# Optimization experiments

Measured on AMD Instinct MI355X. Metric: run time of the kernel, lower is better.

## Reference

```python
import jax, jax.numpy as jnp
import numpy as np

B, C, T, H, W = 8, 512, 8, 28, 28
DI, DO = 256, 512  # dim_inner, dim_out
INIT_STD = 0.01
BN_EPS = 1e-5


def conv1x1(x, w, b):
    # 1x1x1 Conv3d == channel contraction. x: [B,C,T,H,W], w: [O,C], b: [O]
    return jnp.einsum('bcthw,oc->bothw', x, w) + b[None, :, None, None, None]


def setup_inputs() -> dict:
    key = jax.random.key(0)
    ks = jax.random.split(key, 8)
    x = jax.random.normal(ks[0], (B, C, T, H, W), jnp.float32)
    theta_w = INIT_STD * jax.random.normal(ks[1], (DI, C), jnp.float32)
    phi_w = INIT_STD * jax.random.normal(ks[2], (DI, C), jnp.float32)
    g_w = INIT_STD * jax.random.normal(ks[3], (DI, C), jnp.float32)
    out_w = INIT_STD * jax.random.normal(ks[4], (DO, DI), jnp.float32)
    theta_b = jnp.zeros((DI,), jnp.float32)
    phi_b = jnp.zeros((DI,), jnp.float32)
    g_b = jnp.zeros((DI,), jnp.float32)
    out_b = jnp.zeros((DO,), jnp.float32)
    bn_gamma = jnp.ones((DO,), jnp.float32)  # BN_INIT_GAMMA = 1.0
    bn_beta = jnp.zeros((DO,), jnp.float32)
    return {"x": x, "theta_w": theta_w, "theta_b": theta_b, "phi_w": phi_w,
            "phi_b": phi_b, "g_w": g_w, "g_b": g_b, "out_w": out_w,
            "out_b": out_b, "bn_gamma": bn_gamma, "bn_beta": bn_beta}


def reference(x, theta_w, theta_b, phi_w, phi_b, g_w, g_b, out_w, out_b, bn_gamma, bn_beta):
    b, c, t, h, w = x.shape
    scale = DI ** (-0.5)
    # theta on full resolution
    theta = conv1x1(x, theta_w, theta_b).reshape(b, DI, -1)          # [B,DI,N]
    # MaxPool3d((1,2,2)) with stride (1,2,2): H,W even -> block max
    mp = x.reshape(b, c, t, h // 2, 2, w // 2, 2).max(axis=(4, 6))   # [B,C,T,H/2,W/2]
    phi = conv1x1(mp, phi_w, phi_b).reshape(b, DI, -1)               # [B,DI,M]
    g = conv1x1(mp, g_w, g_b).reshape(b, DI, -1)                     # [B,DI,M]
    # attention: theta^T phi -> [B,N,M], scaled softmax over M
    logits = jnp.einsum('bdn,bdm->bnm', theta, phi) * scale
    p = jax.nn.softmax(logits, axis=-1)
    # t = g @ p^T -> [B,DI,N]
    tt = jnp.einsum('bdm,bnm->bdn', g, p).reshape(b, DI, t, h, w)
    out = conv1x1(tt, out_w, out_b)                                  # [B,DO,T,H,W]
    # BatchNorm3d (training-mode batch statistics over B,T,H,W)
    mean = out.mean(axis=(0, 2, 3, 4), keepdims=True)
    var = out.var(axis=(0, 2, 3, 4), keepdims=True)
    out = (out - mean) * jax.lax.rsqrt(var + BN_EPS)
    out = out * bn_gamma[None, :, None, None, None] + bn_beta[None, :, None, None, None]
    return out + x
```

## Files before the change

kernel.cpp:

```cpp
#include <hip/hip_runtime.h>
#include <hip/hip_bf16.h>

#define B_ 8
#define C_ 512
#define T_ 8
#define H_ 28
#define W_ 28
#define N_ (T_*H_*W_)
#define HP_ 14
#define WP_ 14
#define M_ (T_*HP_*WP_)
#define DI_ 256
#define DO_ 512
#define BN_EPS 1e-5f
#define SCALE_LOG2E 0.090168440055560214f
#define PSUM_COLS 392

typedef __attribute__((ext_vector_type(8))) short short8;
typedef __attribute__((ext_vector_type(4))) float float4v;
typedef __attribute__((ext_vector_type(16))) float float16v;
typedef __attribute__((ext_vector_type(2))) float float2v;

__device__ inline unsigned short f2bf(float f) {
    union { float f; unsigned int u; } v; v.f = f;
    unsigned int u = v.u;
    return (unsigned short)((u + 0x7FFFu + ((u >> 16) & 1u)) >> 16);
}
__device__ inline float bf2f(unsigned short h) {
    union { unsigned int u; float f; } v; v.u = ((unsigned int)h) << 16;
    return v.f;
}

__global__ void xpose_x(const float* __restrict__ x, unsigned short* __restrict__ xT) {
    __shared__ float tile[64][65];
    int b = blockIdx.z;
    int c0 = blockIdx.y * 64, n0 = blockIdx.x * 64;
    const float* src = x + (size_t)b * C_ * N_;
    int tx = threadIdx.x & 63, ty = threadIdx.x >> 6;
#pragma unroll
    for (int i = 0; i < 16; i++) {
        int c = ty + i * 4;
        tile[c][tx] = src[(size_t)(c0 + c) * N_ + n0 + tx];
    }
    __syncthreads();
    unsigned short* d = xT + ((size_t)b * N_ + n0) * C_ + c0;
#pragma unroll
    for (int i = 0; i < 16; i++) {
        int n = ty + i * 4;
        d[(size_t)n * C_ + tx] = f2bf(tile[tx][n]);
    }
}

__global__ void pool_xpose(const float* __restrict__ x, unsigned short* __restrict__ mpT) {
    __shared__ unsigned short tile[196][72];
    int b = blockIdx.z, t = blockIdx.y, c0 = blockIdx.x * 64;
    const float* src = x + (((size_t)b * C_ + c0) * T_ + t) * 784;
    for (int idx = threadIdx.x; idx < 64 * 196; idx += 256) {
        int cc = idx / 196, p = idx - cc * 196;
        int hp = p / 14, wp = p - hp * 14;
        const float* r0 = src + (size_t)cc * T_ * 784 + (2 * hp) * 28 + 2 * wp;
        float2v a = *(const float2v*)r0;
        float2v c = *(const float2v*)(r0 + 28);
        float m = fmaxf(fmaxf(a.x, a.y), fmaxf(c.x, c.y));
        tile[p][cc] = f2bf(m);
    }
    __syncthreads();
    unsigned short* d = mpT + ((size_t)b * M_ + t * 196) * C_ + c0;
    for (int idx = threadIdx.x; idx < 196 * 64; idx += 256) {
        int p = idx >> 6, cc = idx & 63;
        d[(size_t)p * C_ + cc] = tile[p][cc];
    }
}

__global__ void cast_w(const float* __restrict__ s, unsigned short* __restrict__ d, int n) {
    int i = blockIdx.x * 256 + threadIdx.x;
    if (i < n) d[i] = f2bf(s[i]);
}

template<int BIAS_MODE>
__global__ __launch_bounds__(256) void btgemm(
        const unsigned short* __restrict__ A, size_t strideAb,
        const unsigned short* __restrict__ Bm, size_t strideBb,
        unsigned short* __restrict__ Dp, size_t strideDb,
        const float* __restrict__ bias, int Mdim, int Ndim, int Kdim) {
    int b = blockIdx.z;
    const unsigned short* Ab = A + (size_t)b * strideAb;
    const unsigned short* Bb = Bm + (size_t)b * strideBb;
    int m0 = blockIdx.x * 64, n0 = blockIdx.y * 64;
    int wave = threadIdx.x >> 6, lane = threadIdx.x & 63;
    int wm = (wave >> 1) * 32, wn = (wave & 1) * 32;
    int lr = lane & 15, lk = lane >> 4;
    float4v acc[2][2] = {};
    for (int k0 = 0; k0 < Kdim; k0 += 32) {
        short8 a[2], bb[2];
#pragma unroll
        for (int i = 0; i < 2; i++) {
            int ar = m0 + wm + i * 16 + lr; if (ar >= Mdim) ar = Mdim - 1;
            a[i] = *(const short8*)(Ab + (size_t)ar * Kdim + k0 + lk * 8);
            int br = n0 + wn + i * 16 + lr; if (br >= Ndim) br = Ndim - 1;
            bb[i] = *(const short8*)(Bb + (size_t)br * Kdim + k0 + lk * 8);
        }
#pragma unroll
        for (int i = 0; i < 2; i++)
#pragma unroll
            for (int j = 0; j < 2; j++)
                acc[i][j] = __builtin_amdgcn_mfma_f32_16x16x32_bf16(a[i], bb[j], acc[i][j], 0, 0, 0);
    }
#pragma unroll
    for (int i = 0; i < 2; i++)
#pragma unroll
        for (int j = 0; j < 2; j++) {
            int col = n0 + wn + j * 16 + lr;
#pragma unroll
            for (int r = 0; r < 4; r++) {
                int row = m0 + wm + i * 16 + lk * 4 + r;
                if (row < Mdim && col < Ndim) {
                    float v = acc[i][j][r];
                    if (BIAS_MODE == 1) v += bias[col];
                    else if (BIAS_MODE == 2) v += bias[row];
                    Dp[(size_t)b * strideDb + (size_t)row * Ndim + col] = f2bf(v);
                }
            }
        }
}

__global__ __launch_bounds__(256, 2) void theta_gemm(
        const unsigned short* __restrict__ xT, const unsigned short* __restrict__ wq,
        unsigned short* __restrict__ thetaT, const float* __restrict__ bias) {
    __shared__ __align__(16) unsigned short wqs[2][32][512];
    const int bid = blockIdx.x;
    const int b = bid & 7;
    const int nblk = bid >> 3;
    const int wave = threadIdx.x >> 6, lane = threadIdx.x & 63;
    const int lr = lane & 15, lk = lane >> 4;
    const unsigned short* Ab = xT + ((size_t)b * N_ + nblk * 128 + wave * 32) * C_;

    short8 a[2][16];
#pragma unroll
    for (int i = 0; i < 2; i++)
#pragma unroll
        for (int kd = 0; kd < 16; kd++)
            a[i][kd] = *(const short8*)(Ab + (size_t)(i * 16 + lr) * C_ + kd * 32 + lk * 8);

    auto stage = [&](int bufi, int t) {
#pragma unroll
        for (int j = 0; j < 8; j++) {
            int row = wave * 8 + j;
            int qq = (lane * 16) ^ ((row & 7) << 4);
            const unsigned short* src = wq + (size_t)(t * 32 + row) * C_ + (qq >> 1);
            unsigned short* dst = &wqs[bufi][0][0] + row * 512;
            __builtin_amdgcn_global_load_lds(
                (const __attribute__((address_space(1))) unsigned int*)src,
                (__attribute__((address_space(3))) unsigned int*)dst, 16, 0, 0);
        }
    };

    stage(0, 0);
    const int hq = (lk * 16) ^ ((lr & 7) << 4);
    unsigned short* D = thetaT + ((size_t)b * N_ + nblk * 128 + wave * 32) * DI_;
    int buf = 0;
#pragma unroll
    for (int t = 0; t < 8; t++) {
        if (t < 7) {
            stage(buf ^ 1, t + 1);
            asm volatile("s_waitcnt vmcnt(8)" ::: "memory");
        } else {
            asm volatile("s_waitcnt vmcnt(0)" ::: "memory");
        }
        __syncthreads();
        const char* W = (const char*)&wqs[buf][0][0];
        float4v acc[2][2] = {};
#pragma unroll
        for (int kd = 0; kd < 16; kd++) {
            short8 b0 = *(const short8*)(W + lr * 1024 + ((kd * 64) ^ hq));
            short8 b1 = *(const short8*)(W + (16 + lr) * 1024 + ((kd * 64) ^ hq));
            acc[0][0] = __builtin_amdgcn_mfma_f32_16x16x32_bf16(a[0][kd], b0, acc[0][0], 0, 0, 0);
            acc[0][1] = __builtin_amdgcn_mfma_f32_16x16x32_bf16(a[0][kd], b1, acc[0][1], 0, 0, 0);
            acc[1][0] = __builtin_amdgcn_mfma_f32_16x16x32_bf16(a[1][kd], b0, acc[1][0], 0, 0, 0);
            acc[1][1] = __builtin_amdgcn_mfma_f32_16x16x32_bf16(a[1][kd], b1, acc[1][1], 0, 0, 0);
        }
#pragma unroll
        for (int i = 0; i < 2; i++)
#pragma unroll
            for (int j = 0; j < 2; j++) {
                int col = t * 32 + j * 16 + lr;
                float bv = bias[col];
#pragma unroll
                for (int r = 0; r < 4; r++) {
                    int row = i * 16 + lk * 4 + r;
                    D[(size_t)row * DI_ + col] = f2bf(acc[i][j][r] + bv);
                }
            }
        __syncthreads();
        buf ^= 1;
    }
}

__global__ __launch_bounds__(256, 2) void out_gemm(
        const unsigned short* __restrict__ wo,
        const unsigned short* __restrict__ Bh, const unsigned short* __restrict__ Bl,
        float* __restrict__ Dp, const float* __restrict__ bias,
        float* __restrict__ psum) {
    __shared__ __align__(16) unsigned short tts[2][2][32][256];
    const int bid = blockIdx.x;
    const int b = bid & 7;
    const int rem = bid >> 3;
    const int doblk = rem & 3;
    const int nchunk = rem >> 2;
    const int wave = threadIdx.x >> 6, lane = threadIdx.x & 63;
    const int lr = lane & 15, lk = lane >> 4;
    const unsigned short* Ab = wo + (size_t)(doblk * 128 + wave * 32) * DI_;
    const unsigned short* BhB = Bh + ((size_t)b * N_ + nchunk * 128) * DI_;
    const unsigned short* BlB = Bl + ((size_t)b * N_ + nchunk * 128) * DI_;

    short8 a[2][8];
#pragma unroll
    for (int i = 0; i < 2; i++)
#pragma unroll
        for (int kd = 0; kd < 8; kd++)
            a[i][kd] = *(const short8*)(Ab + (size_t)(i * 16 + lr) * DI_ + kd * 32 + lk * 8);

    auto stage = [&](int bufi, int t) {
#pragma unroll
        for (int p = 0; p < 2; p++) {
            const unsigned short* S = p ? BlB : BhB;
#pragma unroll
            for (int j = 0; j < 4; j++) {
                int chunk = wave * 4 + j;
                int row = chunk * 2 + (lane >> 5);
                int qq = (((lane & 31) * 16)) ^ ((row & 7) << 4);
                const unsigned short* src = S + (size_t)(t * 32 + row) * DI_ + (qq >> 1);
                unsigned short* dst = &tts[bufi][p][0][0] + chunk * 512;
                __builtin_amdgcn_global_load_lds(
                    (const __attribute__((address_space(1))) unsigned int*)src,
                    (__attribute__((address_space(3))) unsigned int*)dst, 16, 0, 0);
            }
        }
    };

    stage(0, 0);
    const int hq = (lk * 16) ^ ((lr & 7) << 4);
    float4v acc[4][2][2] = {};
    int buf = 0;
#pragma unroll
    for (int t = 0; t < 4; t++) {
        if (t < 3) {
            stage(buf ^ 1, t + 1);
            asm volatile("s_waitcnt vmcnt(8)" ::: "memory");
        } else {
            asm volatile("s_waitcnt vmcnt(0)" ::: "memory");
        }
        __syncthreads();
        const char* th = (const char*)&tts[buf][0][0][0];
        const char* tl = (const char*)&tts[buf][1][0][0];
#pragma unroll
        for (int kd = 0; kd < 8; kd++) {
            short8 bh0 = *(const short8*)(th + lr * 512 + ((kd * 64) ^ hq));
            short8 bh1 = *(const short8*)(th + (16 + lr) * 512 + ((kd * 64) ^ hq));
            short8 bl0 = *(const short8*)(tl + lr * 512 + ((kd * 64) ^ hq));
            short8 bl1 = *(const short8*)(tl + (16 + lr) * 512 + ((kd * 64) ^ hq));
            acc[t][0][0] = __builtin_amdgcn_mfma_f32_16x16x32_bf16(a[0][kd], bh0, acc[t][0][0], 0, 0, 0);
            acc[t][0][0] = __builtin_amdgcn_mfma_f32_16x16x32_bf16(a[0][kd], bl0, acc[t][0][0], 0, 0, 0);
            acc[t][0][1] = __builtin_amdgcn_mfma_f32_16x16x32_bf16(a[0][kd], bh1, acc[t][0][1], 0, 0, 0);
            acc[t][0][1] = __builtin_amdgcn_mfma_f32_16x16x32_bf16(a[0][kd], bl1, acc[t][0][1], 0, 0, 0);
            acc[t][1][0] = __builtin_amdgcn_mfma_f32_16x16x32_bf16(a[1][kd], bh0, acc[t][1][0], 0, 0, 0);
            acc[t][1][0] = __builtin_amdgcn_mfma_f32_16x16x32_bf16(a[1][kd], bl0, acc[t][1][0], 0, 0, 0);
            acc[t][1][1] = __builtin_amdgcn_mfma_f32_16x16x32_bf16(a[1][kd], bh1, acc[t][1][1], 0, 0, 0);
            acc[t][1][1] = __builtin_amdgcn_mfma_f32_16x16x32_bf16(a[1][kd], bl1, acc[t][1][1], 0, 0, 0);
        }
        __syncthreads();
        buf ^= 1;
    }
    float* Db = Dp + (size_t)b * DO_ * N_;
    float s1[2][4] = {}, s2[2][4] = {};
#pragma unroll
    for (int t = 0; t < 4; t++)
#pragma unroll
        for (int i = 0; i < 2; i++)
#pragma unroll
            for (int r = 0; r < 4; r++) {
                int dorow = doblk * 128 + wave * 32 + i * 16 + lk * 4 + r;
                float bv = bias[dorow];
                float v0 = acc[t][i][0][r] + bv;
                float v1 = acc[t][i][1][r] + bv;
                int ncol = nchunk * 128 + t * 32 + lr;
                Db[(size_t)dorow * N_ + ncol] = v0;
                Db[(size_t)dorow * N_ + ncol + 16] = v1;
                s1[i][r] += v0 + v1;
                s2[i][r] += v0 * v0 + v1 * v1;
            }
#pragma unroll
    for (int m = 1; m < 16; m <<= 1)
#pragma unroll
        for (int i = 0; i < 2; i++)
#pragma unroll
            for (int r = 0; r < 4; r++) {
                s1[i][r] += __shfl_xor(s1[i][r], m, 64);
                s2[i][r] += __shfl_xor(s2[i][r], m, 64);
            }
    if (lr == 0) {
        int pcol = b * 49 + nchunk;
#pragma unroll
        for (int i = 0; i < 2; i++)
#pragma unroll
            for (int r = 0; r < 4; r++) {
                int row = doblk * 128 + wave * 32 + i * 16 + lk * 4 + r;
                psum[(size_t)row * PSUM_COLS + pcol] = s1[i][r];
                psum[(size_t)(DO_ + row) * PSUM_COLS + pcol] = s2[i][r];
            }
    }
}

__global__ __launch_bounds__(256, 2) void attn_k(
        const unsigned short* __restrict__ thetaT,
        const unsigned short* __restrict__ phiT,
        const unsigned short* __restrict__ g,
        unsigned short* __restrict__ ttH,
        unsigned short* __restrict__ ttL) {
    __shared__ __align__(16) unsigned short phi_s[2][32][256];
    __shared__ __align__(16) unsigned short g_s[2][256][32];
    const int bid = blockIdx.x;
    const int b = bid & 7;
    const int nblk = bid >> 3;
    const int wave = threadIdx.x >> 6, lane = threadIdx.x & 63;
    const int l31 = lane & 31, hi = lane >> 5;
    const int n0 = nblk * 128 + wave * 32;
    const unsigned short* Q  = thetaT + ((size_t)b * N_ + n0) * DI_;
    const unsigned short* Pg = phiT + (size_t)b * M_ * DI_;
    const unsigned short* G  = g + (size_t)b * DI_ * M_;

    short8 q[16];
#pragma unroll
    for (int kb = 0; kb < 16; kb++)
        q[kb] = *(const short8*)(Q + (size_t)l31 * DI_ + kb * 16 + hi * 8);

    float16v acc[8] = {};
    float rs = 0.f;

    auto stage = [&](int bufi, int t) {
        const unsigned short* phiRow = Pg + (size_t)t * 32 * DI_;
#pragma unroll
        for (int j = 0; j < 4; j++) {
            int chunk = wave * 4 + j;
            int row = chunk * 2 + (lane >> 5);
            int qq = ((lane & 31) * 16) ^ ((row & 7) << 4);
            const unsigned short* src = phiRow + (size_t)row * DI_ + (qq >> 1);
            unsigned short* dst = &phi_s[bufi][0][0] + chunk * 512;
            __builtin_amdgcn_global_load_lds(
                (const __attribute__((address_space(1))) unsigned int*)src,
                (__attribute__((address_space(3))) unsigned int*)dst, 16, 0, 0);
        }
#pragma unroll
        for (int j = 0; j < 4; j++) {
            int chunk = wave * 4 + j;
            int d = chunk * 16 + (lane >> 2);
            int mq = (lane & 3) ^ ((lane >> 3) & 3);
            const unsigned short* src = G + (size_t)d * M_ + t * 32 + mq * 8;
            unsigned short* dst = &g_s[bufi][0][0] + chunk * 512;
            __builtin_amdgcn_global_load_lds(
                (const __attribute__((address_space(1))) unsigned int*)src,
                (__attribute__((address_space(3))) unsigned int*)dst, 16, 0, 0);
        }
    };

    stage(0, 0);
    const int pswz = (l31 & 7) << 4;
    const int gswz = ((lane >> 1) & 3) << 4;
    int buf = 0;
    const int NT = M_ / 32;
    for (int t = 0; t < NT; t++) {
        if (t + 1 < NT) {
            stage(buf ^ 1, t + 1);
            asm volatile("s_waitcnt vmcnt(8)" ::: "memory");
        } else {
            asm volatile("s_waitcnt vmcnt(0)" ::: "memory");
        }
        __syncthreads();

        const char* phiB = (const char*)&phi_s[buf][0][0];
        float16v S = {};
        __builtin_amdgcn_s_setprio(1);
#pragma unroll
        for (int kb = 0; kb < 16; kb++) {
            short8 pha = *(const short8*)(phiB + l31 * 512 + ((kb * 32 + hi * 16) ^ pswz));
            S = __builtin_amdgcn_mfma_f32_32x32x16_bf16(pha, q[kb], S, 0, 0, 0);
        }
        __builtin_amdgcn_s_setprio(0);

        float p[16];
#pragma unroll
        for (int r = 0; r < 16; r++) {
            p[r] = exp2f(S[r] * SCALE_LOG2E);
            rs += p[r];
        }
        unsigned int pk0, pk1, pk2, pk3, pk4, pk5, pk6, pk7;
        asm("v_cvt_pk_bf16_f32 %0, %1, %2" : "=v"(pk0) : "v"(p[0]),  "v"(p[1]));
        asm("v_cvt_pk_bf16_f32 %0, %1, %2" : "=v"(pk1) : "v"(p[2]),  "v"(p[3]));
        asm("v_cvt_pk_bf16_f32 %0, %1, %2" : "=v"(pk2) : "v"(p[4]),  "v"(p[5]));
        asm("v_cvt_pk_bf16_f32 %0, %1, %2" : "=v"(pk3) : "v"(p[6]),  "v"(p[7]));
        asm("v_cvt_pk_bf16_f32 %0, %1, %2" : "=v"(pk4) : "v"(p[8]),  "v"(p[9]));
        asm("v_cvt_pk_bf16_f32 %0, %1, %2" : "=v"(pk5) : "v"(p[10]), "v"(p[11]));
        asm("v_cvt_pk_bf16_f32 %0, %1, %2" : "=v"(pk6) : "v"(p[12]), "v"(p[13]));
        asm("v_cvt_pk_bf16_f32 %0, %1, %2" : "=v"(pk7) : "v"(p[14]), "v"(p[15]));
        asm("v_permlane32_swap_b32 %0, %1" : "+v"(pk0), "+v"(pk2));
        asm("v_permlane32_swap_b32 %0, %1" : "+v"(pk1), "+v"(pk3));
        asm("v_permlane32_swap_b32 %0, %1" : "+v"(pk4), "+v"(pk6));
        asm("v_permlane32_swap_b32 %0, %1" : "+v"(pk5), "+v"(pk7));
        union UF { unsigned int u[4]; short8 s; } pa0, pa1;
        pa0.u[0] = pk0; pa0.u[1] = pk1; pa0.u[2] = pk2; pa0.u[3] = pk3;
        pa1.u[0] = pk4; pa1.u[1] = pk5; pa1.u[2] = pk6; pa1.u[3] = pk7;

        const char* gB = (const char*)&g_s[buf][0][0];
        const int goff0 = (hi * 16) ^ gswz;
        const int goff1 = (32 + hi * 16) ^ gswz;
        __builtin_amdgcn_s_setprio(1);
#pragma unroll
        for (int dblk = 0; dblk < 8; dblk++) {
            short8 gb0 = *(const short8*)(gB + (dblk * 32 + l31) * 64 + goff0);
            short8 gb1 = *(const short8*)(gB + (dblk * 32 + l31) * 64 + goff1);
            acc[dblk] = __builtin_amdgcn_mfma_f32_32x32x16_bf16(pa0.s, gb0, acc[dblk], 0, 0, 0);
            acc[dblk] = __builtin_amdgcn_mfma_f32_32x32x16_bf16(pa1.s, gb1, acc[dblk], 0, 0, 0);
        }
        __builtin_amdgcn_s_setprio(0);
        __syncthreads();
        buf ^= 1;
    }

    rs += __shfl_xor(rs, 32, 64);
    float inv = 1.0f / rs;

    unsigned short* OH = ttH + ((size_t)b * N_ + n0) * DI_;
    unsigned short* OL = ttL + ((size_t)b * N_ + n0) * DI_;
#pragma unroll
    for (int reg = 0; reg < 16; reg++) {
        int n_l = (reg & 3) + 8 * (reg >> 2) + 4 * hi;
        float invn = __shfl(inv, n_l, 64);
#pragma unroll
        for (int dblk = 0; dblk < 8; dblk++) {
            float v = acc[dblk][reg] * invn;
            unsigned short h = f2bf(v);
            unsigned short l = f2bf(v - bf2f(h));
            size_t idx = (size_t)n_l * DI_ + dblk * 32 + l31;
            OH[idx] = h;
            OL[idx] = l;
        }
    }
}

__global__ void bn_finalize(const float* __restrict__ psum, float* __restrict__ stats) {
    int o = blockIdx.x;
    float s = 0.f, q = 0.f;
    for (int c = threadIdx.x; c < PSUM_COLS; c += 256) {
        s += psum[(size_t)o * PSUM_COLS + c];
        q += psum[(size_t)(DO_ + o) * PSUM_COLS + c];
    }
#pragma unroll
    for (int m = 1; m < 64; m <<= 1) { s += __shfl_xor(s, m, 64); q += __shfl_xor(q, m, 64); }
    __shared__ float ws1[4], ws2[4];
    int wave = threadIdx.x >> 6;
    if ((threadIdx.x & 63) == 0) { ws1[wave] = s; ws2[wave] = q; }
    __syncthreads();
    if (threadIdx.x == 0) {
        double S = (double)ws1[0] + ws1[1] + ws1[2] + ws1[3];
        double Q = (double)ws2[0] + ws2[1] + ws2[2] + ws2[3];
        const double cnt = (double)(B_ * N_);
        double mean = S / cnt;
        double var = Q / cnt - mean * mean;
        stats[o] = (float)mean;
        stats[DO_ + o] = (float)(1.0 / sqrt(var + (double)BN_EPS));
    }
}

__global__ void bn_apply(float* __restrict__ out, const float* __restrict__ x,
                         const float* __restrict__ stats, const float* __restrict__ gamma,
                         const float* __restrict__ beta) {
    size_t i = (size_t)blockIdx.x * 256 + threadIdx.x;
    float4v v = ((const float4v*)out)[i];
    float4v xv = ((const float4v*)x)[i];
    int o = (int)((i * 4 / N_) % DO_);
    float mean = stats[o], rsig = stats[DO_ + o];
    float ga = gamma[o], be = beta[o];
    float4v r;
#pragma unroll
    for (int j = 0; j < 4; j++) r[j] = (v[j] - mean) * rsig * ga + be + xv[j];
    ((float4v*)out)[i] = r;
}

extern "C" void kernel_launch(void* const* d_in, const int* in_sizes, int n_in,
                              void* d_out, int out_size, void* d_ws, size_t ws_size,
                              hipStream_t stream) {
    const float* x       = (const float*)d_in[0];
    const float* theta_w = (const float*)d_in[1];
    const float* theta_b = (const float*)d_in[2];
    const float* phi_w   = (const float*)d_in[3];
    const float* phi_b   = (const float*)d_in[4];
    const float* g_w     = (const float*)d_in[5];
    const float* g_b     = (const float*)d_in[6];
    const float* out_w   = (const float*)d_in[7];
    const float* out_b   = (const float*)d_in[8];
    const float* bn_g    = (const float*)d_in[9];
    const float* bn_b    = (const float*)d_in[10];
    float* out = (float*)d_out;

    char* ws = (char*)d_ws;
    size_t off = 0;
    auto alloc = [&](size_t bytes) { void* p = ws + off; off += (bytes + 255) & ~(size_t)255; return p; };
    unsigned short* xT     = (unsigned short*)alloc((size_t)B_ * N_ * C_ * 2);
    unsigned short* mpT    = (unsigned short*)alloc((size_t)B_ * M_ * C_ * 2);
    unsigned short* thetaT = (unsigned short*)alloc((size_t)B_ * N_ * DI_ * 2);
    unsigned short* phiT   = (unsigned short*)alloc((size_t)B_ * M_ * DI_ * 2);
    unsigned short* gbuf   = (unsigned short*)alloc((size_t)B_ * DI_ * M_ * 2);
    unsigned short* wq     = (unsigned short*)alloc((size_t)DI_ * C_ * 2);
    unsigned short* wp     = (unsigned short*)alloc((size_t)DI_ * C_ * 2);
    unsigned short* wg     = (unsigned short*)alloc((size_t)DI_ * C_ * 2);
    unsigned short* wo     = (unsigned short*)alloc((size_t)DO_ * DI_ * 2);
    float* stats           = (float*)alloc((size_t)DO_ * 2 * 4);
    float* psum            = (float*)alloc((size_t)DO_ * 2 * PSUM_COLS * 4);
    unsigned short* ttH    = xT;
    unsigned short* ttL    = xT + (size_t)B_ * N_ * DI_;

    cast_w<<<(DI_ * C_ + 255) / 256, 256, 0, stream>>>(theta_w, wq, DI_ * C_);
    cast_w<<<(DI_ * C_ + 255) / 256, 256, 0, stream>>>(phi_w, wp, DI_ * C_);
    cast_w<<<(DI_ * C_ + 255) / 256, 256, 0, stream>>>(g_w, wg, DI_ * C_);
    cast_w<<<(DO_ * DI_ + 255) / 256, 256, 0, stream>>>(out_w, wo, DO_ * DI_);

    xpose_x<<<dim3(N_ / 64, C_ / 64, B_), 256, 0, stream>>>(x, xT);
    pool_xpose<<<dim3(C_ / 64, T_, B_), 256, 0, stream>>>(x, mpT);

    theta_gemm<<<392, 256, 0, stream>>>(xT, wq, thetaT, theta_b);
    btgemm<1><<<dim3((M_ + 63) / 64, DI_ / 64, B_), 256, 0, stream>>>(
        mpT, (size_t)M_ * C_, wp, 0, phiT, (size_t)M_ * DI_, phi_b, M_, DI_, C_);
    btgemm<2><<<dim3(DI_ / 64, (M_ + 63) / 64, B_), 256, 0, stream>>>(
        wg, 0, mpT, (size_t)M_ * C_, gbuf, (size_t)DI_ * M_, g_b, DI_, M_, C_);

    attn_k<<<dim3((N_ / 128) * 8), 256, 0, stream>>>(thetaT, phiT, gbuf, ttH, ttL);

    out_gemm<<<1568, 256, 0, stream>>>(wo, ttH, ttL, out, out_b, psum);

    bn_finalize<<<DO_, 256, 0, stream>>>(psum, stats);
    bn_apply<<<(size_t)B_ * DO_ * N_ / 4 / 256, 256, 0, stream>>>(out, x, stats, bn_g, bn_b);
}
```

Measured before the change: 383.7 us.

## Replace syncthreads with raw barriers, relax vmcnt waits, split logits accumulator chain

Replaces __syncthreads with a bare s_barrier wrapped in compiler memory fences, which drops the implicit full waitcnt before each barrier. Because the theta GEMM's global stores then stay pending, its vmcnt thresholds are raised so those stores do not force waits. The attention kernel's QK^T MFMA chain is split into two independent accumulators that are summed before the exp. The goal is fewer pipeline stalls from barriers and serial MFMA dependencies. The risks are LDS hazards if the hand-tuned vmcnt counts are wrong, plus a few extra registers.

```diff
diff --git a/kernel.cpp b/kernel.cpp
--- a/kernel.cpp
+++ b/kernel.cpp
@@ -29,6 +29,11 @@
 __device__ inline float bf2f(unsigned short h) {
     union { unsigned int u; float f; } v; v.u = ((unsigned int)h) << 16;
     return v.f;
+}
+__device__ inline void blockbar() {
+    asm volatile("" ::: "memory");
+    __builtin_amdgcn_s_barrier();
+    asm volatile("" ::: "memory");
 }
 
 __global__ void xpose_x(const float* __restrict__ x, unsigned short* __restrict__ xT) {
@@ -163,11 +168,12 @@
     for (int t = 0; t < 8; t++) {
         if (t < 7) {
             stage(buf ^ 1, t + 1);
-            asm volatile("s_waitcnt vmcnt(8)" ::: "memory");
+            if (t == 0) asm volatile("s_waitcnt vmcnt(8)" ::: "memory");
+            else        asm volatile("s_waitcnt vmcnt(24)" ::: "memory");
         } else {
-            asm volatile("s_waitcnt vmcnt(0)" ::: "memory");
-        }
-        __syncthreads();
+            asm volatile("s_waitcnt vmcnt(16)" ::: "memory");
+        }
+        blockbar();
         const char* W = (const char*)&wqs[buf][0][0];
         float4v acc[2][2] = {};
 #pragma unroll
@@ -191,7 +197,7 @@
                     D[(size_t)row * DI_ + col] = f2bf(acc[i][j][r] + bv);
                 }
             }
-        __syncthreads();
+        blockbar();
         buf ^= 1;
     }
 }
@@ -250,7 +256,7 @@
         } else {
             asm volatile("s_waitcnt vmcnt(0)" ::: "memory");
         }
-        __syncthreads();
+        blockbar();
         const char* th = (const char*)&tts[buf][0][0][0];
         const char* tl = (const char*)&tts[buf][1][0][0];
 #pragma unroll
@@ -268,7 +274,7 @@
             acc[t][1][1] = __builtin_amdgcn_mfma_f32_16x16x32_bf16(a[1][kd], bh1, acc[t][1][1], 0, 0, 0);
             acc[t][1][1] = __builtin_amdgcn_mfma_f32_16x16x32_bf16(a[1][kd], bl1, acc[t][1][1], 0, 0, 0);
         }
-        __syncthreads();
+        blockbar();
         buf ^= 1;
     }
     float* Db = Dp + (size_t)b * DO_ * N_;
@@ -375,22 +381,24 @@
         } else {
             asm volatile("s_waitcnt vmcnt(0)" ::: "memory");
         }
-        __syncthreads();
+        blockbar();
 
         const char* phiB = (const char*)&phi_s[buf][0][0];
-        float16v S = {};
+        float16v S0 = {}, S1 = {};
         __builtin_amdgcn_s_setprio(1);
 #pragma unroll
-        for (int kb = 0; kb < 16; kb++) {
-            short8 pha = *(const short8*)(phiB + l31 * 512 + ((kb * 32 + hi * 16) ^ pswz));
-            S = __builtin_amdgcn_mfma_f32_32x32x16_bf16(pha, q[kb], S, 0, 0, 0);
+        for (int kb = 0; kb < 8; kb++) {
+            short8 pha0 = *(const short8*)(phiB + l31 * 512 + ((kb * 32 + hi * 16) ^ pswz));
+            short8 pha1 = *(const short8*)(phiB + l31 * 512 + (((kb + 8) * 32 + hi * 16) ^ pswz));
+            S0 = __builtin_amdgcn_mfma_f32_32x32x16_bf16(pha0, q[kb], S0, 0, 0, 0);
+            S1 = __builtin_amdgcn_mfma_f32_32x32x16_bf16(pha1, q[kb + 8], S1, 0, 0, 0);
         }
         __builtin_amdgcn_s_setprio(0);
 
         float p[16];
 #pragma unroll
         for (int r = 0; r < 16; r++) {
-            p[r] = exp2f(S[r] * SCALE_LOG2E);
+            p[r] = exp2f((S0[r] + S1[r]) * SCALE_LOG2E);
             rs += p[r];
         }
         unsigned int pk0, pk1, pk2, pk3, pk4, pk5, pk6, pk7;
@@ -422,7 +430,7 @@
             acc[dblk] = __builtin_amdgcn_mfma_f32_32x32x16_bf16(pa1.s, gb1, acc[dblk], 0, 0, 0);
         }
         __builtin_amdgcn_s_setprio(0);
-        __syncthreads();
+        blockbar();
         buf ^= 1;
     }
 
```

After: 398.8 us. 3.9% more time.
